# Performance work log

Measured on AMD Instinct MI355X. Metric: run time of the kernel, lower is better.

## Reference

```python
import jax, jax.numpy as jnp
import numpy as np

B, CIN, F, H, W = 4, 256, 128, 64, 64
EPS = 1e-5

def _conv1x1(x, Wm, b):
    # x: [B,C,H,W], Wm: [O,C] (1x1 conv kernel), b: [O]
    return jnp.einsum('bchw,oc->bohw', x, Wm) + b[None, :, None, None]

def setup_inputs() -> dict:
    key = jax.random.key(0)
    ks = jax.random.split(key, 11)
    s_in = 1.0 / np.sqrt(CIN)
    s_f = 1.0 / np.sqrt(F)
    return {
        'x':    jax.random.normal(ks[0], (B, CIN, H, W), jnp.float32),
        'Wg':   jax.random.normal(ks[1], (F, CIN), jnp.float32) * s_in,
        'bg':   jax.random.normal(ks[2], (F,), jnp.float32) * s_in,
        'Wt':   jax.random.normal(ks[3], (F, CIN), jnp.float32) * s_in,
        'bt':   jax.random.normal(ks[4], (F,), jnp.float32) * s_in,
        'Wp':   jax.random.normal(ks[5], (F, CIN), jnp.float32) * s_in,
        'bp':   jax.random.normal(ks[6], (F,), jnp.float32) * s_in,
        'Wz':   jax.random.normal(ks[7], (CIN, F), jnp.float32) * s_f,
        'bz':   jax.random.normal(ks[8], (CIN,), jnp.float32) * s_f,
        'ln_w': jax.random.normal(ks[9], (CIN, H, W), jnp.float32) * 0.1,
        'ln_b': jax.random.normal(ks[10], (CIN, H, W), jnp.float32) * 0.1,
    }

def reference(x, Wg, bg, Wt, bt, Wp, bp, Wz, bz, ln_w, ln_b):
    b, _, h, w = x.shape
    n = h * w
    # 1x1 conv projections
    g = _conv1x1(x, Wg, bg).reshape(b, F, n).transpose(0, 2, 1)      # [B,N,F]
    theta = _conv1x1(x, Wt, bt).reshape(b, F, n).transpose(0, 2, 1)  # [B,N,F]
    phi = _conv1x1(x, Wp, bp).reshape(b, F, n)                        # [B,F,N]
    # embedded-Gaussian affinity + softmax attention
    f = jnp.einsum('bnf,bfm->bnm', theta, phi)                        # [B,N,N]
    attn = jax.nn.softmax(f, axis=-1)
    y = jnp.einsum('bnm,bmf->bnf', attn, g)                           # [B,N,F]
    y = y.transpose(0, 2, 1).reshape(b, F, h, w)                      # [B,F,H,W]
    # output projection
    z = _conv1x1(y, Wz, bz)                                           # [B,CIN,H,W]
    # LayerNorm over (C,H,W) per sample, affine params shaped [C,H,W]
    mu = jnp.mean(z, axis=(1, 2, 3), keepdims=True)
    var = jnp.var(z, axis=(1, 2, 3), keepdims=True)
    z = (z - mu) * jax.lax.rsqrt(var + EPS)
    z = z * ln_w[None] + ln_b[None]
    return z + x
```

## Files before the change

### kernel.cpp

```cpp
#include <hip/hip_runtime.h>
#include <stdint.h>

#define CIN 256
#define FDIM 128
#define NSP 4096
#define EPS 1e-5f

typedef __attribute__((ext_vector_type(8))) short short8;
typedef __attribute__((ext_vector_type(4))) float f32x4;
typedef __attribute__((ext_vector_type(16))) float f32x16;

__device__ __forceinline__ short f2bf(float f) {
  union { float f; uint32_t u; } v; v.f = f;
  uint32_t r = v.u + 0x7fffu + ((v.u >> 16) & 1u);
  return (short)(r >> 16);
}
__device__ __forceinline__ float bf2f(short h) {
  union { uint32_t u; float f; } v; v.u = ((uint32_t)(uint16_t)h) << 16;
  return v.f;
}

__global__ void prep_weights(const float* __restrict__ Wg, const float* __restrict__ Wt,
                             const float* __restrict__ Wp, const float* __restrict__ Wz,
                             short* __restrict__ Wbf, short* __restrict__ Wzbf) {
  int idx = blockIdx.x * 256 + threadIdx.x;
  if (idx < 384 * 256) {
    int row = idx >> 8, col = idx & 255;
    float v;
    if (row < 128)       v = Wt[row * 256 + col];
    else if (row < 256)  v = Wp[(row - 128) * 256 + col];
    else                 v = Wg[(row - 256) * 256 + col];
    Wbf[idx] = f2bf(v);
  } else {
    int j = idx - 384 * 256;
    if (j < 256 * 128) Wzbf[j] = f2bf(Wz[j]);
  }
}

__global__ void prep_xT(const float* __restrict__ x, short* __restrict__ xT) {
  __shared__ float tile[32][33];
  int b = blockIdx.z, c0 = blockIdx.y * 32, n0 = blockIdx.x * 32;
  int r = threadIdx.x >> 5, c = threadIdx.x & 31;
  const float* xb = x + (size_t)b * CIN * NSP;
#pragma unroll
  for (int k = 0; k < 4; k++)
    tile[r + 8 * k][c] = xb[(size_t)(c0 + r + 8 * k) * NSP + n0 + c];
  __syncthreads();
  short* xTb = xT + (size_t)b * NSP * CIN;
#pragma unroll
  for (int k = 0; k < 4; k++)
    xTb[(size_t)(n0 + r + 8 * k) * CIN + c0 + c] = f2bf(tile[c][r + 8 * k]);
}

__global__ void __launch_bounds__(256)
proj_kernel(const short* __restrict__ xT, const short* __restrict__ Wbf,
            const float* __restrict__ bt, const float* __restrict__ bp,
            const float* __restrict__ bg,
            short* __restrict__ theta, short* __restrict__ Kb, short* __restrict__ gT) {
  __shared__ short lds[5120];
  int bx = blockIdx.x;
  int b = bx >> 7;
  int n0 = (bx & 127) << 5;
  int p = blockIdx.y;
  int t = threadIdx.x, w = t >> 6, lane = t & 63, l15 = lane & 15, quad = lane >> 4;

  const short* arow = xT + (size_t)(b * NSP + n0 + (w & 1) * 16 + l15) * CIN;
  short8 a[8];
#pragma unroll
  for (int s = 0; s < 8; s++) a[s] = *(const short8*)(arow + s * 32 + quad * 8);

  const short* Wsrc = Wbf + p * 128 * 256;
  f32x4 zero = {0.f, 0.f, 0.f, 0.f};
  f32x4 acc[4];
#pragma unroll
  for (int i = 0; i < 4; i++) acc[i] = zero;

#pragma unroll
  for (int s = 0; s < 8; s++) {
#pragma unroll
    for (int ft = 0; ft < 4; ft++) {
      int ftg = (w >> 1) * 4 + ft;
      short8 bfr = *(const short8*)(Wsrc + (ftg * 16 + l15) * 256 + s * 32 + quad * 8);
      acc[ft] = __builtin_amdgcn_mfma_f32_16x16x32_bf16(a[s], bfr, acc[ft], 0, 0, 0);
    }
  }

  const float* bias = (p == 0) ? bt : (p == 1) ? bp : bg;
  if (p < 2) {
#pragma unroll
    for (int ft = 0; ft < 4; ft++) {
      int ftg = (w >> 1) * 4 + ft;
      float bv = bias[ftg * 16 + l15];
#pragma unroll
      for (int rr = 0; rr < 4; rr++) {
        int n = (w & 1) * 16 + quad * 4 + rr;
        lds[n * 136 + ftg * 16 + l15] = f2bf(acc[ft][rr] + bv);
      }
    }
    __syncthreads();
    short* dst = ((p == 0) ? theta : Kb) + (size_t)(b * NSP + n0) * FDIM;
#pragma unroll
    for (int i = 0; i < 2; i++) {
      int flat = t + 256 * i;
      int row = flat >> 4, ch = flat & 15;
      *(short8*)(dst + (size_t)row * FDIM + ch * 8) = *(const short8*)(lds + row * 136 + ch * 8);
    }
  } else {
#pragma unroll
    for (int ft = 0; ft < 4; ft++) {
      int ftg = (w >> 1) * 4 + ft;
      float bv = bias[ftg * 16 + l15];
#pragma unroll
      for (int rr = 0; rr < 4; rr++) {
        int n = (w & 1) * 16 + quad * 4 + rr;
        lds[(ftg * 16 + l15) * 40 + n] = f2bf(acc[ft][rr] + bv);
      }
    }
    __syncthreads();
    short* dst = gT + (size_t)b * FDIM * NSP + n0;
#pragma unroll
    for (int i = 0; i < 2; i++) {
      int flat = t + 256 * i;
      int f = flat >> 2, c = flat & 3;
      *(short8*)(dst + (size_t)f * NSP + c * 8) = *(const short8*)(lds + f * 40 + c * 8);
    }
  }
}

__global__ void __launch_bounds__(256, 2)
flash_kernel(const short* __restrict__ thetab, const short* __restrict__ Kb,
             const short* __restrict__ gT, short* __restrict__ opart,
             float* __restrict__ lpart) {
  __shared__ __attribute__((aligned(16))) char smem[75776];

  const int bx = blockIdx.x;
  const int b  = bx >> 7;
  const int r  = bx & 127;
  const int q0 = (r >> 2) << 7;
  const int kc = r & 3;
  const int t = threadIdx.x, w = t >> 6, lane = t & 63;
  const int l31 = lane & 31, h = lane >> 5;
  const int qw = q0 + w * 32;

  const short* Qsrc = thetab + (size_t)b * NSP * FDIM;
  const short* Ksrc = Kb + (size_t)b * NSP * FDIM;
  const short* Vsrc = gT + (size_t)b * FDIM * NSP;

  short8 qf[8];
#pragma unroll
  for (int s = 0; s < 8; s++)
    qf[s] = *(const short8*)(Qsrc + (size_t)(qw + l31) * FDIM + s * 16 + h * 8);

  f32x16 O[4];
#pragma unroll
  for (int i = 0; i < 4; i++)
#pragma unroll
    for (int j = 0; j < 16; j++) O[i][j] = 0.f;
  float lsum = 0.f;

  const int kr0 = t >> 4, kcc0 = t & 15;
  const int kr1 = 16 + (t >> 4);
  const int vf0 = t >> 2, vcc0 = t & 3;
  const int vf1 = 64 + (t >> 2);

  const int kA0 = kc << 10;
  short8 rKa0, rKa1, rKb0, rKb1, rVa0, rVa1, rVb0, rVb1;

  {
    rKa0 = *(const short8*)(Ksrc + (size_t)(kA0 + kr0) * FDIM + kcc0 * 8);
    rKa1 = *(const short8*)(Ksrc + (size_t)(kA0 + kr1) * FDIM + kcc0 * 8);
    rKb0 = *(const short8*)(Ksrc + (size_t)(kA0 + 32 + kr0) * FDIM + kcc0 * 8);
    rKb1 = *(const short8*)(Ksrc + (size_t)(kA0 + 32 + kr1) * FDIM + kcc0 * 8);
    rVa0 = *(const short8*)(Vsrc + (size_t)vf0 * NSP + kA0 + vcc0 * 8);
    rVa1 = *(const short8*)(Vsrc + (size_t)vf1 * NSP + kA0 + vcc0 * 8);
    rVb0 = *(const short8*)(Vsrc + (size_t)vf0 * NSP + kA0 + 32 + vcc0 * 8);
    rVb1 = *(const short8*)(Vsrc + (size_t)vf1 * NSP + kA0 + 32 + vcc0 * 8);
    short* Ka = (short*)(smem);
    short* Kbd = (short*)(smem + 8704);
    short* Va = (short*)(smem + 17408);
    short* Vb = (short*)(smem + 27648);
    *(short8*)(Ka + kr0 * 136 + kcc0 * 8) = rKa0;
    *(short8*)(Ka + kr1 * 136 + kcc0 * 8) = rKa1;
    *(short8*)(Kbd + kr0 * 136 + kcc0 * 8) = rKb0;
    *(short8*)(Kbd + kr1 * 136 + kcc0 * 8) = rKb1;
    *(short8*)(Va + vf0 * 40 + vcc0 * 8) = rVa0;
    *(short8*)(Va + vf1 * 40 + vcc0 * 8) = rVa1;
    *(short8*)(Vb + vf0 * 40 + vcc0 * 8) = rVb0;
    *(short8*)(Vb + vf1 * 40 + vcc0 * 8) = rVb1;
  }

#pragma unroll 2
  for (int it = 0; it < 16; ++it) {
    __syncthreads();
    if (it < 15) {
      int kk = kA0 + (it + 1) * 64;
      rKa0 = *(const short8*)(Ksrc + (size_t)(kk + kr0) * FDIM + kcc0 * 8);
      rKa1 = *(const short8*)(Ksrc + (size_t)(kk + kr1) * FDIM + kcc0 * 8);
      rKb0 = *(const short8*)(Ksrc + (size_t)(kk + 32 + kr0) * FDIM + kcc0 * 8);
      rKb1 = *(const short8*)(Ksrc + (size_t)(kk + 32 + kr1) * FDIM + kcc0 * 8);
      rVa0 = *(const short8*)(Vsrc + (size_t)vf0 * NSP + kk + vcc0 * 8);
      rVa1 = *(const short8*)(Vsrc + (size_t)vf1 * NSP + kk + vcc0 * 8);
      rVb0 = *(const short8*)(Vsrc + (size_t)vf0 * NSP + kk + 32 + vcc0 * 8);
      rVb1 = *(const short8*)(Vsrc + (size_t)vf1 * NSP + kk + 32 + vcc0 * 8);
    }
    const char* bufc = smem + (it & 1) * 37888;
    const short* Kla = (const short*)(bufc);
    const short* Klb = (const short*)(bufc + 8704);
    const short* Vla = (const short*)(bufc + 17408);
    const short* Vlb = (const short*)(bufc + 27648);

    f32x16 S0, S1;
#pragma unroll
    for (int j = 0; j < 16; j++) { S0[j] = 0.f; S1[j] = 0.f; }
    __builtin_amdgcn_s_setprio(1);
#pragma unroll
    for (int s = 0; s < 8; s++) {
      short8 ak0 = *(const short8*)(Kla + l31 * 136 + s * 16 + h * 8);
      short8 ak1 = *(const short8*)(Klb + l31 * 136 + s * 16 + h * 8);
      S0 = __builtin_amdgcn_mfma_f32_32x32x16_bf16(ak0, qf[s], S0, 0, 0, 0);
      S1 = __builtin_amdgcn_mfma_f32_32x32x16_bf16(ak1, qf[s], S1, 0, 0, 0);
    }
    __builtin_amdgcn_s_setprio(0);

    short8 AfA[2], AfB[2];
#pragma unroll
    for (int sub = 0; sub < 2; sub++) {
      float p[16];
#pragma unroll
      for (int i = 0; i < 16; i++) p[i] = __expf(sub ? S1[i] : S0[i]);
      float t8[8];
#pragma unroll
      for (int i = 0; i < 8; i++) t8[i] = p[2 * i] + p[2 * i + 1];
      lsum += ((t8[0] + t8[1]) + (t8[2] + t8[3])) + ((t8[4] + t8[5]) + (t8[6] + t8[7]));

      uint32_t W[8];
#pragma unroll
      for (int j = 0; j < 8; j++)
        asm("v_cvt_pk_bf16_f32 %0, %1, %2" : "=v"(W[j]) : "v"(p[2 * j]), "v"(p[2 * j + 1]));
      asm("v_permlane32_swap_b32 %0, %1" : "+v"(W[0]), "+v"(W[2]));
      asm("v_permlane32_swap_b32 %0, %1" : "+v"(W[1]), "+v"(W[3]));
      asm("v_permlane32_swap_b32 %0, %1" : "+v"(W[4]), "+v"(W[6]));
      asm("v_permlane32_swap_b32 %0, %1" : "+v"(W[5]), "+v"(W[7]));
      union { short8 s; uint32_t u[4]; } u0, u1;
      u0.u[0] = W[0]; u0.u[1] = W[1]; u0.u[2] = W[2]; u0.u[3] = W[3];
      u1.u[0] = W[4]; u1.u[1] = W[5]; u1.u[2] = W[6]; u1.u[3] = W[7];
      if (sub) { AfB[0] = u0.s; AfB[1] = u1.s; }
      else     { AfA[0] = u0.s; AfA[1] = u1.s; }
    }

    __builtin_amdgcn_s_setprio(1);
#pragma unroll
    for (int ft = 0; ft < 4; ft++) {
#pragma unroll
      for (int tt = 0; tt < 2; tt++) {
        short8 bva = *(const short8*)(Vla + (ft * 32 + l31) * 40 + tt * 16 + h * 8);
        O[ft] = __builtin_amdgcn_mfma_f32_32x32x16_bf16(AfA[tt], bva, O[ft], 0, 0, 0);
        short8 bvb = *(const short8*)(Vlb + (ft * 32 + l31) * 40 + tt * 16 + h * 8);
        O[ft] = __builtin_amdgcn_mfma_f32_32x32x16_bf16(AfB[tt], bvb, O[ft], 0, 0, 0);
      }
    }
    __builtin_amdgcn_s_setprio(0);

    if (it < 15) {
      char* nb = smem + ((it + 1) & 1) * 37888;
      short* Ka = (short*)(nb);
      short* Kbd = (short*)(nb + 8704);
      short* Va = (short*)(nb + 17408);
      short* Vb = (short*)(nb + 27648);
      *(short8*)(Ka + kr0 * 136 + kcc0 * 8) = rKa0;
      *(short8*)(Ka + kr1 * 136 + kcc0 * 8) = rKa1;
      *(short8*)(Kbd + kr0 * 136 + kcc0 * 8) = rKb0;
      *(short8*)(Kbd + kr1 * 136 + kcc0 * 8) = rKb1;
      *(short8*)(Va + vf0 * 40 + vcc0 * 8) = rVa0;
      *(short8*)(Va + vf1 * 40 + vcc0 * 8) = rVa1;
      *(short8*)(Vb + vf0 * 40 + vcc0 * 8) = rVb0;
      *(short8*)(Vb + vf1 * 40 + vcc0 * 8) = rVb1;
    }
  }

  lsum += __shfl_xor(lsum, 32, 64);

  __syncthreads();
  short* tr = (short*)smem + w * 32 * 136;
#pragma unroll
  for (int ft = 0; ft < 4; ft++) {
#pragma unroll
    for (int reg = 0; reg < 16; reg++) {
      int rowq = (reg & 3) + 8 * (reg >> 2) + 4 * h;
      tr[rowq * 136 + ft * 32 + l31] = f2bf(O[ft][reg]);
    }
  }
  short* od = opart + ((size_t)(kc * 4 + b) * NSP + qw) * FDIM;
#pragma unroll
  for (int i = 0; i < 8; i++) {
    int slot = lane + 64 * i;
    int row = slot >> 4, c = slot & 15;
    *(short8*)(od + (size_t)row * FDIM + c * 8) = *(const short8*)(tr + row * 136 + c * 8);
  }
  if (h == 0) lpart[(size_t)(kc * 4 + b) * NSP + qw + l31] = lsum;
}

__global__ void __launch_bounds__(256)
zproj_kernel(const short* __restrict__ opart, const float* __restrict__ lpart,
             const short* __restrict__ Wzbf, const float* __restrict__ bz,
             short* __restrict__ zb, float* __restrict__ psums) {
  __shared__ short ldsT[128 * 40];
  __shared__ float wsum[4][2];
  int bx = blockIdx.x;
  int b = bx >> 7;
  int n0 = (bx & 127) << 5;
  int ch0 = blockIdx.y * 128;
  int t = threadIdx.x, w = t >> 6, lane = t & 63, l15 = lane & 15, quad = lane >> 4;

  int row = n0 + (w & 1) * 16 + l15;
  float L = 0.f;
#pragma unroll
  for (int kcc = 0; kcc < 4; kcc++) L += lpart[(size_t)(kcc * 4 + b) * NSP + row];
  float inv = 1.0f / L;

  short8 a[4];
#pragma unroll
  for (int s = 0; s < 4; s++) {
    float accv[8] = {0, 0, 0, 0, 0, 0, 0, 0};
#pragma unroll
    for (int kcc = 0; kcc < 4; kcc++) {
      short8 v = *(const short8*)(opart + ((size_t)(kcc * 4 + b) * NSP + row) * FDIM + s * 32 + quad * 8);
#pragma unroll
      for (int j = 0; j < 8; j++) accv[j] += bf2f(v[j]);
    }
    short8 av;
#pragma unroll
    for (int j = 0; j < 8; j++) av[j] = f2bf(accv[j] * inv);
    a[s] = av;
  }

  f32x4 zero = {0.f, 0.f, 0.f, 0.f};
  f32x4 acc[4];
#pragma unroll
  for (int i = 0; i < 4; i++) acc[i] = zero;
#pragma unroll
  for (int s = 0; s < 4; s++) {
#pragma unroll
    for (int ct = 0; ct < 4; ct++) {
      int co = ch0 + (w >> 1) * 64 + ct * 16 + l15;
      short8 bfr = *(const short8*)(Wzbf + (size_t)co * FDIM + s * 32 + quad * 8);
      acc[ct] = __builtin_amdgcn_mfma_f32_16x16x32_bf16(a[s], bfr, acc[ct], 0, 0, 0);
    }
  }

  float s1 = 0.0f, s2 = 0.0f;
#pragma unroll
  for (int ct = 0; ct < 4; ct++) {
    int cg = (w >> 1) * 64 + ct * 16 + l15;
    float bv = bz[ch0 + cg];
#pragma unroll
    for (int rr = 0; rr < 4; rr++) {
      float v = acc[ct][rr] + bv;
      s1 += v; s2 += v * v;
      ldsT[cg * 40 + (w & 1) * 16 + quad * 4 + rr] = f2bf(v);
    }
  }
#pragma unroll
  for (int off = 32; off >= 1; off >>= 1) {
    s1 += __shfl_xor(s1, off, 64);
    s2 += __shfl_xor(s2, off, 64);
  }
  if (lane == 0) { wsum[w][0] = s1; wsum[w][1] = s2; }
  __syncthreads();
  if (t == 0) {
    int bid = blockIdx.y * 512 + bx;
    psums[bid * 2] = wsum[0][0] + wsum[1][0] + wsum[2][0] + wsum[3][0];
    psums[bid * 2 + 1] = wsum[0][1] + wsum[1][1] + wsum[2][1] + wsum[3][1];
  }
  short* dst = zb + (size_t)b * CIN * NSP + (size_t)ch0 * NSP + n0;
#pragma unroll
  for (int i = 0; i < 2; i++) {
    int flat = t + 256 * i;
    int c = flat >> 2, ch = flat & 3;
    *(short8*)(dst + (size_t)c * NSP + ch * 8) = *(const short8*)(ldsT + c * 40 + ch * 8);
  }
}

__global__ void reduce_sums(const float* __restrict__ psums, float* __restrict__ sums) {
  __shared__ float red[8];
  int t = threadIdx.x;
  if (t < 8) red[t] = 0.f;
  __syncthreads();
  for (int i = t; i < 1024; i += 256) {
    int b = (i & 511) >> 7;
    atomicAdd(&red[b * 2], psums[i * 2]);
    atomicAdd(&red[b * 2 + 1], psums[i * 2 + 1]);
  }
  __syncthreads();
  if (t < 8) sums[t] = red[t];
}

__global__ void __launch_bounds__(256)
finalize_kernel(const short* __restrict__ zbuf, const float* __restrict__ x,
                const float* __restrict__ lnw, const float* __restrict__ lnb,
                const float* __restrict__ sums, float* __restrict__ out) {
  int gid = blockIdx.x * 256 + threadIdx.x;
  size_t e0 = (size_t)gid * 8;
  int b = (int)(e0 >> 20);
  size_t ib = e0 & ((size_t)(1u << 20) - 1);
  float mean = sums[b * 2] * (1.0f / 1048576.0f);
  float var = sums[b * 2 + 1] * (1.0f / 1048576.0f) - mean * mean;
  float rs = rsqrtf(var + EPS);
  short8 zv = *(const short8*)(zbuf + e0);
#pragma unroll
  for (int k = 0; k < 8; k++) {
    float z = bf2f(zv[k]);
    out[e0 + k] = (z - mean) * rs * lnw[ib + k] + lnb[ib + k] + x[e0 + k];
  }
}

extern "C" void kernel_launch(void* const* d_in, const int* in_sizes, int n_in,
                              void* d_out, int out_size, void* d_ws, size_t ws_size,
                              hipStream_t stream) {
  const float* x   = (const float*)d_in[0];
  const float* Wg  = (const float*)d_in[1];
  const float* bg  = (const float*)d_in[2];
  const float* Wt  = (const float*)d_in[3];
  const float* bt  = (const float*)d_in[4];
  const float* Wp  = (const float*)d_in[5];
  const float* bp  = (const float*)d_in[6];
  const float* Wz  = (const float*)d_in[7];
  const float* bz  = (const float*)d_in[8];
  const float* lnw = (const float*)d_in[9];
  const float* lnb = (const float*)d_in[10];
  float* out = (float*)d_out;

  char* ws = (char*)d_ws;
  short* Wbf    = (short*)(ws);
  short* Wzbf   = (short*)(ws + 196608);
  short* xT     = (short*)(ws + 262144);
  short* opart  = (short*)(ws + 262144);
  float* lpart  = (float*)(ws + 17039360);
  short* thetab = (short*)(ws + 17301504);
  short* Kb     = (short*)(ws + 21495808);
  short* gT     = (short*)(ws + 25690112);
  short* zb     = (short*)(ws + 17301504);
  float* sums   = (float*)(ws + 29884416);
  float* psums  = (float*)(ws + 29884448);

  prep_weights<<<512, 256, 0, stream>>>(Wg, Wt, Wp, Wz, Wbf, Wzbf);
  prep_xT<<<dim3(128, 8, 4), 256, 0, stream>>>(x, xT);
  proj_kernel<<<dim3(512, 3), 256, 0, stream>>>(xT, Wbf, bt, bp, bg, thetab, Kb, gT);
  flash_kernel<<<512, 256, 0, stream>>>(thetab, Kb, gT, opart, lpart);
  zproj_kernel<<<dim3(512, 2), 256, 0, stream>>>(opart, lpart, Wzbf, bz, zb, psums);
  reduce_sums<<<1, 256, 0, stream>>>(psums, sums);
  finalize_kernel<<<2048, 256, 0, stream>>>(zb, x, lnw, lnb, sums, out);
}
```

Before: 193.4 us.

## Stream V from global into registers, swizzle K LDS, merge prep and reduce kernels

The flash kernel stops staging V in LDS. Each wave now loads its V fragments straight from global memory into registers every iteration, and only K stays double-buffered in LDS, using an XOR swizzle in place of padding. This shrinks shared memory enough that launch_bounds can request 4 blocks per CU instead of 2. The two prep kernels are also merged into one launch, and the separate reduce_sums kernel is replaced by atomicAdd in zproj, removing two kernel launches. The risks are exposed global-load latency for V inside the loop, higher register pressure from holding 16 short8 V fragments, and atomic contention plus order-dependent float summation.

```diff
diff --git a/kernel.cpp b/kernel.cpp
--- a/kernel.cpp
+++ b/kernel.cpp
@@ -20,36 +20,41 @@
   return v.f;
 }
 
-__global__ void prep_weights(const float* __restrict__ Wg, const float* __restrict__ Wt,
-                             const float* __restrict__ Wp, const float* __restrict__ Wz,
-                             short* __restrict__ Wbf, short* __restrict__ Wzbf) {
-  int idx = blockIdx.x * 256 + threadIdx.x;
-  if (idx < 384 * 256) {
-    int row = idx >> 8, col = idx & 255;
-    float v;
-    if (row < 128)       v = Wt[row * 256 + col];
-    else if (row < 256)  v = Wp[(row - 128) * 256 + col];
-    else                 v = Wg[(row - 256) * 256 + col];
-    Wbf[idx] = f2bf(v);
+__global__ void prep_all(const float* __restrict__ x,
+                         const float* __restrict__ Wg, const float* __restrict__ Wt,
+                         const float* __restrict__ Wp, const float* __restrict__ Wz,
+                         short* __restrict__ xT, short* __restrict__ Wbf,
+                         short* __restrict__ Wzbf, float* __restrict__ sums) {
+  __shared__ float tile[32][33];
+  int bx = blockIdx.x;
+  if (bx < 4096) {
+    int b = bx >> 10, c0 = ((bx >> 7) & 7) * 32, n0 = (bx & 127) * 32;
+    int r = threadIdx.x >> 5, c = threadIdx.x & 31;
+    const float* xb = x + (size_t)b * CIN * NSP;
+#pragma unroll
+    for (int k = 0; k < 4; k++)
+      tile[r + 8 * k][c] = xb[(size_t)(c0 + r + 8 * k) * NSP + n0 + c];
+    __syncthreads();
+    short* xTb = xT + (size_t)b * NSP * CIN;
+#pragma unroll
+    for (int k = 0; k < 4; k++)
+      xTb[(size_t)(n0 + r + 8 * k) * CIN + c0 + c] = f2bf(tile[c][r + 8 * k]);
   } else {
-    int j = idx - 384 * 256;
-    if (j < 256 * 128) Wzbf[j] = f2bf(Wz[j]);
-  }
-}
-
-__global__ void prep_xT(const float* __restrict__ x, short* __restrict__ xT) {
-  __shared__ float tile[32][33];
-  int b = blockIdx.z, c0 = blockIdx.y * 32, n0 = blockIdx.x * 32;
-  int r = threadIdx.x >> 5, c = threadIdx.x & 31;
-  const float* xb = x + (size_t)b * CIN * NSP;
-#pragma unroll
-  for (int k = 0; k < 4; k++)
-    tile[r + 8 * k][c] = xb[(size_t)(c0 + r + 8 * k) * NSP + n0 + c];
-  __syncthreads();
-  short* xTb = xT + (size_t)b * NSP * CIN;
-#pragma unroll
-  for (int k = 0; k < 4; k++)
-    xTb[(size_t)(n0 + r + 8 * k) * CIN + c0 + c] = f2bf(tile[c][r + 8 * k]);
+    int wb = bx - 4096;
+    if (wb == 0 && threadIdx.x < 8) sums[threadIdx.x] = 0.f;
+    int idx = wb * 256 + threadIdx.x;
+    if (idx < 384 * 256) {
+      int row = idx >> 8, col = idx & 255;
+      float v;
+      if (row < 128)       v = Wt[row * 256 + col];
+      else if (row < 256)  v = Wp[(row - 128) * 256 + col];
+      else                 v = Wg[(row - 256) * 256 + col];
+      Wbf[idx] = f2bf(v);
+    } else {
+      int j = idx - 384 * 256;
+      if (j < 256 * 128) Wzbf[j] = f2bf(Wz[j]);
+    }
+  }
 }
 
 __global__ void __launch_bounds__(256)
@@ -127,11 +132,11 @@
   }
 }
 
-__global__ void __launch_bounds__(256, 2)
+__global__ void __launch_bounds__(256, 4)
 flash_kernel(const short* __restrict__ thetab, const short* __restrict__ Kb,
              const short* __restrict__ gT, short* __restrict__ opart,
              float* __restrict__ lpart) {
-  __shared__ __attribute__((aligned(16))) char smem[75776];
+  __shared__ __attribute__((aligned(16))) char smem[34816];
 
   const int bx = blockIdx.x;
   const int b  = bx >> 7;
@@ -159,55 +164,49 @@
   float lsum = 0.f;
 
   const int kr0 = t >> 4, kcc0 = t & 15;
-  const int kr1 = 16 + (t >> 4);
-  const int vf0 = t >> 2, vcc0 = t & 3;
-  const int vf1 = 64 + (t >> 2);
+  const int kr1 = kr0 + 16;
+  const int wo0 = kcc0 * 256 + ((kr0 ^ (kcc0 & 7)) * 8);
+  const int wo1 = kcc0 * 256 + ((kr1 ^ (kcc0 & 7)) * 8);
 
   const int kA0 = kc << 10;
-  short8 rKa0, rKa1, rKb0, rKb1, rVa0, rVa1, rVb0, rVb1;
+  short8 rKa0, rKa1, rKb0, rKb1;
 
   {
     rKa0 = *(const short8*)(Ksrc + (size_t)(kA0 + kr0) * FDIM + kcc0 * 8);
     rKa1 = *(const short8*)(Ksrc + (size_t)(kA0 + kr1) * FDIM + kcc0 * 8);
     rKb0 = *(const short8*)(Ksrc + (size_t)(kA0 + 32 + kr0) * FDIM + kcc0 * 8);
     rKb1 = *(const short8*)(Ksrc + (size_t)(kA0 + 32 + kr1) * FDIM + kcc0 * 8);
-    rVa0 = *(const short8*)(Vsrc + (size_t)vf0 * NSP + kA0 + vcc0 * 8);
-    rVa1 = *(const short8*)(Vsrc + (size_t)vf1 * NSP + kA0 + vcc0 * 8);
-    rVb0 = *(const short8*)(Vsrc + (size_t)vf0 * NSP + kA0 + 32 + vcc0 * 8);
-    rVb1 = *(const short8*)(Vsrc + (size_t)vf1 * NSP + kA0 + 32 + vcc0 * 8);
-    short* Ka = (short*)(smem);
-    short* Kbd = (short*)(smem + 8704);
-    short* Va = (short*)(smem + 17408);
-    short* Vb = (short*)(smem + 27648);
-    *(short8*)(Ka + kr0 * 136 + kcc0 * 8) = rKa0;
-    *(short8*)(Ka + kr1 * 136 + kcc0 * 8) = rKa1;
-    *(short8*)(Kbd + kr0 * 136 + kcc0 * 8) = rKb0;
-    *(short8*)(Kbd + kr1 * 136 + kcc0 * 8) = rKb1;
-    *(short8*)(Va + vf0 * 40 + vcc0 * 8) = rVa0;
-    *(short8*)(Va + vf1 * 40 + vcc0 * 8) = rVa1;
-    *(short8*)(Vb + vf0 * 40 + vcc0 * 8) = rVb0;
-    *(short8*)(Vb + vf1 * 40 + vcc0 * 8) = rVb1;
+    short* K0 = (short*)smem;
+    *(short8*)(K0 + wo0) = rKa0;
+    *(short8*)(K0 + wo1) = rKa1;
+    *(short8*)(K0 + 4096 + wo0) = rKb0;
+    *(short8*)(K0 + 4096 + wo1) = rKb1;
   }
 
 #pragma unroll 2
   for (int it = 0; it < 16; ++it) {
     __syncthreads();
+    const int kk = kA0 + it * 64;
+
+    short8 rV[16];
+#pragma unroll
+    for (int sub = 0; sub < 2; sub++)
+#pragma unroll
+      for (int ft = 0; ft < 4; ft++)
+#pragma unroll
+        for (int tt = 0; tt < 2; tt++)
+          rV[sub * 8 + ft * 2 + tt] =
+              *(const short8*)(Vsrc + (size_t)(ft * 32 + l31) * NSP + kk + sub * 32 + tt * 16 + h * 8);
+
     if (it < 15) {
-      int kk = kA0 + (it + 1) * 64;
-      rKa0 = *(const short8*)(Ksrc + (size_t)(kk + kr0) * FDIM + kcc0 * 8);
-      rKa1 = *(const short8*)(Ksrc + (size_t)(kk + kr1) * FDIM + kcc0 * 8);
-      rKb0 = *(const short8*)(Ksrc + (size_t)(kk + 32 + kr0) * FDIM + kcc0 * 8);
-      rKb1 = *(const short8*)(Ksrc + (size_t)(kk + 32 + kr1) * FDIM + kcc0 * 8);
-      rVa0 = *(const short8*)(Vsrc + (size_t)vf0 * NSP + kk + vcc0 * 8);
-      rVa1 = *(const short8*)(Vsrc + (size_t)vf1 * NSP + kk + vcc0 * 8);
-      rVb0 = *(const short8*)(Vsrc + (size_t)vf0 * NSP + kk + 32 + vcc0 * 8);
-      rVb1 = *(const short8*)(Vsrc + (size_t)vf1 * NSP + kk + 32 + vcc0 * 8);
-    }
-    const char* bufc = smem + (it & 1) * 37888;
-    const short* Kla = (const short*)(bufc);
-    const short* Klb = (const short*)(bufc + 8704);
-    const short* Vla = (const short*)(bufc + 17408);
-    const short* Vlb = (const short*)(bufc + 27648);
+      int kn = kk + 64;
+      rKa0 = *(const short8*)(Ksrc + (size_t)(kn + kr0) * FDIM + kcc0 * 8);
+      rKa1 = *(const short8*)(Ksrc + (size_t)(kn + kr1) * FDIM + kcc0 * 8);
+      rKb0 = *(const short8*)(Ksrc + (size_t)(kn + 32 + kr0) * FDIM + kcc0 * 8);
+      rKb1 = *(const short8*)(Ksrc + (size_t)(kn + 32 + kr1) * FDIM + kcc0 * 8);
+    }
+
+    const short* Kl = (const short*)(smem + (it & 1) * 16384);
 
     f32x16 S0, S1;
 #pragma unroll
@@ -215,8 +214,10 @@
     __builtin_amdgcn_s_setprio(1);
 #pragma unroll
     for (int s = 0; s < 8; s++) {
-      short8 ak0 = *(const short8*)(Kla + l31 * 136 + s * 16 + h * 8);
-      short8 ak1 = *(const short8*)(Klb + l31 * 136 + s * 16 + h * 8);
+      int c = 2 * s + h;
+      const short* base = Kl + c * 256 + ((l31 ^ (c & 7)) * 8);
+      short8 ak0 = *(const short8*)(base);
+      short8 ak1 = *(const short8*)(base + 4096);
       S0 = __builtin_amdgcn_mfma_f32_32x32x16_bf16(ak0, qf[s], S0, 0, 0, 0);
       S1 = __builtin_amdgcn_mfma_f32_32x32x16_bf16(ak1, qf[s], S1, 0, 0, 0);
     }
@@ -253,28 +254,18 @@
     for (int ft = 0; ft < 4; ft++) {
 #pragma unroll
       for (int tt = 0; tt < 2; tt++) {
-        short8 bva = *(const short8*)(Vla + (ft * 32 + l31) * 40 + tt * 16 + h * 8);
-        O[ft] = __builtin_amdgcn_mfma_f32_32x32x16_bf16(AfA[tt], bva, O[ft], 0, 0, 0);
-        short8 bvb = *(const short8*)(Vlb + (ft * 32 + l31) * 40 + tt * 16 + h * 8);
-        O[ft] = __builtin_amdgcn_mfma_f32_32x32x16_bf16(AfB[tt], bvb, O[ft], 0, 0, 0);
+        O[ft] = __builtin_amdgcn_mfma_f32_32x32x16_bf16(AfA[tt], rV[ft * 2 + tt], O[ft], 0, 0, 0);
+        O[ft] = __builtin_amdgcn_mfma_f32_32x32x16_bf16(AfB[tt], rV[8 + ft * 2 + tt], O[ft], 0, 0, 0);
       }
     }
     __builtin_amdgcn_s_setprio(0);
 
     if (it < 15) {
-      char* nb = smem + ((it + 1) & 1) * 37888;
-      short* Ka = (short*)(nb);
-      short* Kbd = (short*)(nb + 8704);
-      short* Va = (short*)(nb + 17408);
-      short* Vb = (short*)(nb + 27648);
-      *(short8*)(Ka + kr0 * 136 + kcc0 * 8) = rKa0;
-      *(short8*)(Ka + kr1 * 136 + kcc0 * 8) = rKa1;
-      *(short8*)(Kbd + kr0 * 136 + kcc0 * 8) = rKb0;
-      *(short8*)(Kbd + kr1 * 136 + kcc0 * 8) = rKb1;
-      *(short8*)(Va + vf0 * 40 + vcc0 * 8) = rVa0;
-      *(short8*)(Va + vf1 * 40 + vcc0 * 8) = rVa1;
-      *(short8*)(Vb + vf0 * 40 + vcc0 * 8) = rVb0;
-      *(short8*)(Vb + vf1 * 40 + vcc0 * 8) = rVb1;
+      short* Kd = (short*)(smem + ((it + 1) & 1) * 16384);
+      *(short8*)(Kd + wo0) = rKa0;
+      *(short8*)(Kd + wo1) = rKa1;
+      *(short8*)(Kd + 4096 + wo0) = rKb0;
+      *(short8*)(Kd + 4096 + wo1) = rKb1;
     }
   }
 
@@ -303,7 +294,7 @@
 __global__ void __launch_bounds__(256)
 zproj_kernel(const short* __restrict__ opart, const float* __restrict__ lpart,
              const short* __restrict__ Wzbf, const float* __restrict__ bz,
-             short* __restrict__ zb, float* __restrict__ psums) {
+             short* __restrict__ zb, float* __restrict__ sums) {
   __shared__ short ldsT[128 * 40];
   __shared__ float wsum[4][2];
   int bx = blockIdx.x;
@@ -368,9 +359,8 @@
   if (lane == 0) { wsum[w][0] = s1; wsum[w][1] = s2; }
   __syncthreads();
   if (t == 0) {
-    int bid = blockIdx.y * 512 + bx;
-    psums[bid * 2] = wsum[0][0] + wsum[1][0] + wsum[2][0] + wsum[3][0];
-    psums[bid * 2 + 1] = wsum[0][1] + wsum[1][1] + wsum[2][1] + wsum[3][1];
+    atomicAdd(&sums[b * 2],     wsum[0][0] + wsum[1][0] + wsum[2][0] + wsum[3][0]);
+    atomicAdd(&sums[b * 2 + 1], wsum[0][1] + wsum[1][1] + wsum[2][1] + wsum[3][1]);
   }
   short* dst = zb + (size_t)b * CIN * NSP + (size_t)ch0 * NSP + n0;
 #pragma unroll
@@ -379,20 +369,6 @@
     int c = flat >> 2, ch = flat & 3;
     *(short8*)(dst + (size_t)c * NSP + ch * 8) = *(const short8*)(ldsT + c * 40 + ch * 8);
   }
-}
-
-__global__ void reduce_sums(const float* __restrict__ psums, float* __restrict__ sums) {
-  __shared__ float red[8];
-  int t = threadIdx.x;
-  if (t < 8) red[t] = 0.f;
-  __syncthreads();
-  for (int i = t; i < 1024; i += 256) {
-    int b = (i & 511) >> 7;
-    atomicAdd(&red[b * 2], psums[i * 2]);
-    atomicAdd(&red[b * 2 + 1], psums[i * 2 + 1]);
-  }
-  __syncthreads();
-  if (t < 8) sums[t] = red[t];
 }
 
 __global__ void __launch_bounds__(256)
@@ -441,13 +417,10 @@
   short* gT     = (short*)(ws + 25690112);
   short* zb     = (short*)(ws + 17301504);
   float* sums   = (float*)(ws + 29884416);
-  float* psums  = (float*)(ws + 29884448);
-
-  prep_weights<<<512, 256, 0, stream>>>(Wg, Wt, Wp, Wz, Wbf, Wzbf);
-  prep_xT<<<dim3(128, 8, 4), 256, 0, stream>>>(x, xT);
+
+  prep_all<<<4608, 256, 0, stream>>>(x, Wg, Wt, Wp, Wz, xT, Wbf, Wzbf, sums);
   proj_kernel<<<dim3(512, 3), 256, 0, stream>>>(xT, Wbf, bt, bp, bg, thetab, Kb, gT);
   flash_kernel<<<512, 256, 0, stream>>>(thetab, Kb, gT, opart, lpart);
-  zproj_kernel<<<dim3(512, 2), 256, 0, stream>>>(opart, lpart, Wzbf, bz, zb, psums);
-  reduce_sums<<<1, 256, 0, stream>>>(psums, sums);
+  zproj_kernel<<<dim3(512, 2), 256, 0, stream>>>(opart, lpart, Wzbf, bz, zb, sums);
   finalize_kernel<<<2048, 256, 0, stream>>>(zb, x, lnw, lnb, sums, out);
 }
```

Measured after the change: 535.4 us. 177% more time.
